# Performance work log

Measured on AMD Instinct MI355X. Metric: run time of the kernel, lower is better.

## Reference

```python
import jax, jax.numpy as jnp
import numpy as np

B, S, D, E = 2, 2048, 1024, 8
H = 2 * D          # hidden_dim = 2*n_embd
A = H // 16        # adapt_dim


def _ln(x, g, b):
    m = x.mean(-1, keepdims=True)
    v = x.var(-1, keepdims=True)
    return (x - m) * jax.lax.rsqrt(v + 1e-5) * g + b


def setup_inputs() -> dict:
    key = jax.random.key(0)
    ks = jax.random.split(key, 16)
    s = 1.0 / np.sqrt(D)        # shared-linear init scale
    sa = s * 0.01               # adapter-linear init scale
    sg = 0.01 / np.sqrt(A)      # expert adapter init scale
    f32 = jnp.float32
    return {
        "x": jax.random.normal(ks[0], (B, S, D), f32),
        "expert_weights": jax.nn.softmax(jax.random.normal(ks[1], (B * S, E), f32), -1),
        "up_w": jax.random.normal(ks[2], (H, D), f32) * s,
        "gate_w": jax.random.normal(ks[3], (H, D), f32) * s,
        "down_w": jax.random.normal(ks[4], (D, H), f32) * s,
        "pre_w": jax.random.normal(ks[5], (A, D), f32) * sa,
        "post_w": jax.random.normal(ks[6], (A, H), f32) * sa,
        "an_g": jnp.ones((A,), f32),
        "an_b": jnp.zeros((A,), f32),
        "adapt_proj_w": jax.random.normal(ks[7], (H, A), f32) * sa,
        "adapter_w": jax.random.normal(ks[8], (E, A, A), f32) * sg,
        "adapter_g": jnp.ones((E, A), f32),
        "adapter_b": jnp.zeros((E, A), f32),
        "expert_proj_w": jax.random.normal(ks[9], (H, A), f32) * sg,
        "output_proj_w": jax.random.normal(ks[10], (D, H), f32) * sg,
    }


def reference(x, expert_weights, up_w, gate_w, down_w, pre_w, post_w, an_g, an_b,
              adapt_proj_w, adapter_w, adapter_g, adapter_b, expert_proj_w, output_proj_w):
    # ---- SharedExpertMLP ----
    up = x @ up_w.T                                  # [B,S,H]
    gate = x @ gate_w.T                              # [B,S,H]
    hidden = jax.nn.silu(gate) * up                  # SwiGLU
    adapt_in = _ln(x @ pre_w.T, an_g, an_b)          # [B,S,A]
    adapt_out = _ln(hidden @ post_w.T, an_g, an_b)   # [B,S,A]
    w = jnp.einsum('bsa,bta->bst', adapt_in, adapt_out)
    w = jax.nn.silu(jnp.clip(w, -5.0, 5.0))          # clamp+SiLU score
    # explicit fp32 bmm as in original autocast-disabled block
    adapt = jnp.einsum('bst,bta->bsa',
                       w.astype(jnp.float32),
                       adapt_in.astype(jnp.float32)).astype(x.dtype)
    hidden = hidden + 0.1 * (adapt @ adapt_proj_w.T)
    shared_out = hidden @ down_w.T                   # [B,S,D] (dropout is identity in eval)

    # ---- per-token expert mixing ----
    xf = x.reshape(-1, x.shape[-1])                  # [N,D], N=B*S
    a = _ln(xf @ pre_w.T, an_g, an_b)                # [N,A]
    h = jnp.einsum('na,eca->nec', a, adapter_w)      # per-expert low-rank adapt [N,E,A]
    h = _ln(h, adapter_g[None], adapter_b[None])
    mixed = jnp.einsum('ne,nea->na', expert_weights, h)   # combine experts [N,A]
    out = (mixed @ expert_proj_w.T) @ output_proj_w.T     # [N,D]
    return shared_out + out.reshape(x.shape)
```

## Files before the change

### kernel.cpp

```cpp
#include <hip/hip_runtime.h>
#include <hip/hip_bf16.h>
#include <math.h>

#define Bq 2
#define Sq 2048
#define Dq 1024
#define Eq 8
#define Hq 2048
#define Aq 128
#define Nq (Bq*Sq)

typedef __attribute__((ext_vector_type(4))) float f32x4;
typedef __attribute__((ext_vector_type(8))) short bfrag;

__device__ __forceinline__ float silu_f(float x) {
    return x / (1.0f + expf(-x));
}
__device__ __forceinline__ unsigned short f2bf(float x) {
    unsigned u = __float_as_uint(x);
    u += 0x7fffu + ((u >> 16) & 1u);
    return (unsigned short)(u >> 16);
}
__device__ __forceinline__ float bf2f(unsigned short h) {
    return __uint_as_float(((unsigned)h) << 16);
}
__device__ __forceinline__ void gl16(const unsigned short* g, unsigned short* l) {
    __builtin_amdgcn_global_load_lds(
        (const __attribute__((address_space(1))) void*)g,
        (__attribute__((address_space(3))) void*)(void*)l, 16, 0, 0);
}

#define WAITV_BAR(N)                                            \
    asm volatile("s_waitcnt vmcnt(" #N ")" ::: "memory");       \
    __builtin_amdgcn_s_barrier();                               \
    asm volatile("" ::: "memory")
#define END_BAR()                                               \
    asm volatile("" ::: "memory");                              \
    __builtin_amdgcn_s_barrier();                               \
    asm volatile("" ::: "memory")
#define WAITV(N) asm volatile("s_waitcnt vmcnt(" #N ")" ::: "memory")
#define BARF()                                                  \
    asm volatile("" ::: "memory");                              \
    __builtin_amdgcn_s_barrier();                               \
    asm volatile("" ::: "memory")

__global__ __launch_bounds__(256)
void convert_all(const float* __restrict__ x,  const float* __restrict__ gw,
                 const float* __restrict__ uw, const float* __restrict__ dw,
                 const float* __restrict__ pw, const float* __restrict__ ow,
                 const float* __restrict__ opw, const float* __restrict__ aw,
                 const float* __restrict__ apw, const float* __restrict__ epw,
                 unsigned short* xh,  unsigned short* gwh, unsigned short* uwh,
                 unsigned short* dwh, unsigned short* pwh, unsigned short* powh,
                 unsigned short* oph, unsigned short* adw, unsigned short* apT)
{
    __shared__ float t[32][33];
    if (blockIdx.x >= 2048) {
        int bid = blockIdx.x - 2048;
        int z   = bid >> 8;
        int rem = bid & 255;
        int bx  = rem & 3, by = rem >> 2;
        const float* in = z ? epw : apw;
        unsigned short* out = apT + (size_t)z * Hq * Aq;
        int tx = threadIdx.x & 31, ty = threadIdx.x >> 5;
        int r0 = by * 32, c0 = bx * 32;
#pragma unroll
        for (int j = 0; j < 4; j++)
            t[ty + j * 8][tx] = in[(size_t)(r0 + ty + j * 8) * Aq + c0 + tx];
        __syncthreads();
#pragma unroll
        for (int j = 0; j < 4; j++)
            out[(size_t)(c0 + ty + j * 8) * Hq + r0 + tx] = f2bf(t[tx][ty + j * 8]);
        return;
    }
    const int T = 3276800;
    for (int i = blockIdx.x * 256 + threadIdx.x; i < T; i += 2048 * 256) {
        const float* in; unsigned short* hi; int j = i;
        if (j < 1048576)                 { in = x;   hi = xh;  }
        else if ((j -= 1048576) < 524288){ in = gw;  hi = gwh; }
        else if ((j -= 524288) < 524288) { in = uw;  hi = uwh; }
        else if ((j -= 524288) < 524288) { in = dw;  hi = dwh; }
        else if ((j -= 524288) < 32768)  { in = pw;  hi = pwh; }
        else if ((j -= 32768) < 65536)   { in = ow;  hi = powh; }
        else if ((j -= 65536) < 524288)  { in = opw; hi = oph; }
        else { j -= 524288;                in = aw;  hi = adw; }
        float4 v = ((const float4*)in)[j];
        ((ushort4*)hi)[j] = make_ushort4(f2bf(v.x), f2bf(v.y), f2bf(v.z), f2bf(v.w));
    }
}

template<int EPI>
__global__ __launch_bounds__(512)
void mg(const unsigned short* __restrict__ Ah, const unsigned short* __restrict__ Bh,
        void* __restrict__ Cv, int N, int K, int kchunks,
        long zA, long zB, long zC, long pz)
{
    __shared__ __align__(16) unsigned short lds[32768];

    const int tid = threadIdx.x;
    const int l   = tid & 63;
    const int w   = tid >> 6;
    const int wr  = w >> 2, wc = w & 3;
    const int bm0 = blockIdx.y * 128, bn0 = blockIdx.x * 128;
    const int bz  = blockIdx.z / kchunks;
    const int kz  = blockIdx.z - bz * kchunks;
    const int kcnt = K / kchunks;
    const int kbeg = kz * kcnt;
    const int kend = kbeg + kcnt;

    const unsigned short* A0 = Ah + (size_t)bz * zA;
    const unsigned short* B0 = Bh + (size_t)bz * zB;

    const int srow = tid >> 3;
    const int sq   = (tid & 7) ^ (srow & 7);
    const size_t aoff = (size_t)(bm0 + srow) * K + sq * 8;
    const size_t boff = (size_t)(bn0 + srow) * K + sq * 8;
    const size_t r64  = (size_t)64 * K;

    auto stage = [&](int b, int kt) {
        unsigned short* d = &lds[b * 16384 + (w << 9)];
        gl16(A0 + aoff + kt,       d + 0);
        gl16(A0 + aoff + kt + r64, d + 4096);
        gl16(B0 + boff + kt,       d + 8192);
        gl16(B0 + boff + kt + r64, d + 12288);
    };

    const int rowa = (wr * 64 + (l & 15)) * 64;
    const int rowb = (wc * 32 + (l & 15)) * 64;
    const int q0 = (((l >> 4)    ) ^ (l & 7)) << 3;
    const int q1 = (((l >> 4) + 4) ^ (l & 7)) << 3;

    f32x4 acc[4][2];
#pragma unroll
    for (int i = 0; i < 4; i++)
#pragma unroll
        for (int j = 0; j < 2; j++) acc[i][j] = (f32x4){0.f, 0.f, 0.f, 0.f};

    stage(0, kbeg);
    int cur = 0;
    for (int kt = kbeg; kt < kend; kt += 64) {
        if (kt + 64 < kend) {
            stage(cur ^ 1, kt + 64);
            WAITV_BAR(4);
        } else {
            WAITV_BAR(0);
        }
        const int cb = cur * 16384;
#pragma unroll
        for (int ks = 0; ks < 2; ks++) {
            const int qo = ks ? q1 : q0;
            bfrag a4[4], b4[2];
#pragma unroll
            for (int f = 0; f < 4; f++)
                a4[f] = *(const bfrag*)&lds[cb + rowa + f * 1024 + qo];
#pragma unroll
            for (int f = 0; f < 2; f++)
                b4[f] = *(const bfrag*)&lds[cb + 8192 + rowb + f * 1024 + qo];
#pragma unroll
            for (int i = 0; i < 4; i++)
#pragma unroll
                for (int j = 0; j < 2; j++)
                    acc[i][j] = __builtin_amdgcn_mfma_f32_16x16x32_bf16(a4[i], b4[j], acc[i][j], 0, 0, 0);
        }
        END_BAR();
        cur ^= 1;
    }

    const int crow0 = bm0 + wr * 64 + (l >> 4) * 4;
    const int ccol0 = bn0 + wc * 32 + (l & 15);
#pragma unroll
    for (int i = 0; i < 4; i++)
#pragma unroll
        for (int j = 0; j < 2; j++)
#pragma unroll
            for (int r = 0; r < 4; r++) {
                size_t idx = (size_t)(crow0 + i * 16 + r) * N + (ccol0 + j * 16);
                float v = acc[i][j][r];
                if (EPI == 0)
                    ((float*)Cv + (size_t)bz * zC + (size_t)kz * pz)[idx] = v;
                else if (EPI == 1)
                    ((unsigned short*)Cv + (size_t)bz * zC)[idx] =
                        f2bf(silu_f(fminf(fmaxf(v, -5.f), 5.f)));
                else
                    ((unsigned short*)Cv + (size_t)bz * zC)[idx] = f2bf(v);
            }
}

__global__ __launch_bounds__(512)
void mgpair(const unsigned short* __restrict__ dwh, const unsigned short* __restrict__ apT,
            float* __restrict__ kdp,
            const unsigned short* __restrict__ xh, const unsigned short* __restrict__ pwh,
            float* __restrict__ p1)
{
    __shared__ __align__(16) unsigned short lds[32768];

    const int tid = threadIdx.x;
    const int l   = tid & 63;
    const int w   = tid >> 6;
    const int wr  = w >> 2, wc = w & 3;

    const unsigned short *Ah, *Bh; float* Cv;
    int K, kchunks, by, zidx;
    long zA, zB, zC, pz;
    int bid = blockIdx.x;
    if (bid < 256) {
        Ah = dwh; Bh = apT; Cv = kdp; K = Hq; kchunks = 16;
        zA = (long)Dq * Hq; zB = (long)Aq * Hq; zC = (long)16 * Dq * Aq; pz = (long)Dq * Aq;
        by = bid & 7; zidx = bid >> 3;
    } else {
        int r = bid - 256;
        Ah = xh; Bh = pwh; Cv = p1; K = Dq; kchunks = 8;
        zA = 0; zB = 0; zC = 0; pz = (long)Nq * Aq;
        by = r & 31; zidx = r >> 5;
    }
    const int N = Aq;
    const int bm0 = by * 128, bn0 = 0;
    const int bz  = zidx / kchunks;
    const int kz  = zidx - bz * kchunks;
    const int kcnt = K / kchunks;
    const int kbeg = kz * kcnt;
    const int kend = kbeg + kcnt;

    const unsigned short* A0 = Ah + (size_t)bz * zA;
    const unsigned short* B0 = Bh + (size_t)bz * zB;

    const int srow = tid >> 3;
    const int sq   = (tid & 7) ^ (srow & 7);
    const size_t aoff = (size_t)(bm0 + srow) * K + sq * 8;
    const size_t boff = (size_t)(bn0 + srow) * K + sq * 8;
    const size_t r64  = (size_t)64 * K;

    auto stage = [&](int b, int kt) {
        unsigned short* d = &lds[b * 16384 + (w << 9)];
        gl16(A0 + aoff + kt,       d + 0);
        gl16(A0 + aoff + kt + r64, d + 4096);
        gl16(B0 + boff + kt,       d + 8192);
        gl16(B0 + boff + kt + r64, d + 12288);
    };

    const int rowa = (wr * 64 + (l & 15)) * 64;
    const int rowb = (wc * 32 + (l & 15)) * 64;
    const int q0 = (((l >> 4)    ) ^ (l & 7)) << 3;
    const int q1 = (((l >> 4) + 4) ^ (l & 7)) << 3;

    f32x4 acc[4][2];
#pragma unroll
    for (int i = 0; i < 4; i++)
#pragma unroll
        for (int j = 0; j < 2; j++) acc[i][j] = (f32x4){0.f, 0.f, 0.f, 0.f};

    stage(0, kbeg);
    int cur = 0;
    for (int kt = kbeg; kt < kend; kt += 64) {
        if (kt + 64 < kend) {
            stage(cur ^ 1, kt + 64);
            WAITV_BAR(4);
        } else {
            WAITV_BAR(0);
        }
        const int cb = cur * 16384;
#pragma unroll
        for (int ks = 0; ks < 2; ks++) {
            const int qo = ks ? q1 : q0;
            bfrag a4[4], b4[2];
#pragma unroll
            for (int f = 0; f < 4; f++)
                a4[f] = *(const bfrag*)&lds[cb + rowa + f * 1024 + qo];
#pragma unroll
            for (int f = 0; f < 2; f++)
                b4[f] = *(const bfrag*)&lds[cb + 8192 + rowb + f * 1024 + qo];
#pragma unroll
            for (int i = 0; i < 4; i++)
#pragma unroll
                for (int j = 0; j < 2; j++)
                    acc[i][j] = __builtin_amdgcn_mfma_f32_16x16x32_bf16(a4[i], b4[j], acc[i][j], 0, 0, 0);
        }
        END_BAR();
        cur ^= 1;
    }

    const int crow0 = bm0 + wr * 64 + (l >> 4) * 4;
    const int ccol0 = bn0 + wc * 32 + (l & 15);
    float* C = Cv + (size_t)bz * zC + (size_t)kz * pz;
#pragma unroll
    for (int i = 0; i < 4; i++)
#pragma unroll
        for (int j = 0; j < 2; j++)
#pragma unroll
            for (int r = 0; r < 4; r++)
                C[(size_t)(crow0 + i * 16 + r) * N + (ccol0 + j * 16)] = acc[i][j][r];
}

__global__ __launch_bounds__(512)
void gsc(const unsigned short* __restrict__ ainh, const unsigned short* __restrict__ aouth,
         const unsigned short* __restrict__ ainT, float* __restrict__ p3)
{
    __shared__ __align__(16) unsigned short lds[65536];
    const int AIN = 0, AOUT = 16384, AINT = 32768, PB = 49152;

    const int tid = threadIdx.x;
    const int l   = tid & 63;
    const int w   = tid >> 6;
    const int wr  = w >> 2, wc = w & 3;
    const int tz  = blockIdx.x;
    const int ib  = blockIdx.y;
    const int b   = blockIdx.z;
    const long SA = (long)Sq * Aq;

    auto stage32 = [&](int base, const unsigned short* src, size_t kstride) {
#pragma unroll
        for (int rd = 0; rd < 4; rd++) {
            int grow = rd * 32 + (w << 2) + (l >> 4);
            int slot = (l & 15) ^ (grow & 15);
            gl16(src + (size_t)grow * kstride + slot * 8,
                 &lds[base + rd * 4096 + (w << 9)]);
        }
    };

    const unsigned short* ainI_src = ainh + (size_t)b * SA + (size_t)(ib * 128) * Aq;
    f32x4 acc2[4][2];
#pragma unroll
    for (int i = 0; i < 4; i++)
#pragma unroll
        for (int j = 0; j < 2; j++) acc2[i][j] = (f32x4){0.f, 0.f, 0.f, 0.f};

    {
        int tglob = tz * 2;
        stage32(AIN,  ainI_src, Aq);
        stage32(AOUT, aouth + (size_t)b * SA + (size_t)(tglob * 128) * Aq, Aq);
        stage32(AINT, ainT  + (size_t)b * SA + (size_t)(tglob * 128), Sq);
        WAITV_BAR(0);
    }

    const int rowa = (wr * 64 + (l & 15)) * 128;
    const int rowb = (wc * 32 + (l & 15)) * 128;

#pragma unroll 1
    for (int t = 0; t < 2; t++) {
        if (t == 1) {
            int tglob = tz * 2 + 1;
            stage32(AOUT, aouth + (size_t)b * SA + (size_t)(tglob * 128) * Aq, Aq);
            stage32(AINT, ainT  + (size_t)b * SA + (size_t)(tglob * 128), Sq);
            WAITV_BAR(0);
        }
        f32x4 acc1[4][2];
#pragma unroll
        for (int i = 0; i < 4; i++)
#pragma unroll
            for (int j = 0; j < 2; j++) acc1[i][j] = (f32x4){0.f, 0.f, 0.f, 0.f};
#pragma unroll
        for (int ks = 0; ks < 4; ks++) {
            const int qo = ((ks * 4 + (l >> 4)) ^ (l & 15)) << 3;
            bfrag a4[4], b4[2];
#pragma unroll
            for (int f = 0; f < 4; f++)
                a4[f] = *(const bfrag*)&lds[AIN + rowa + f * 2048 + qo];
#pragma unroll
            for (int f = 0; f < 2; f++)
                b4[f] = *(const bfrag*)&lds[AOUT + rowb + f * 2048 + qo];
#pragma unroll
            for (int i = 0; i < 4; i++)
#pragma unroll
                for (int j = 0; j < 2; j++)
                    acc1[i][j] = __builtin_amdgcn_mfma_f32_16x16x32_bf16(a4[i], b4[j], acc1[i][j], 0, 0, 0);
        }
        {
            const int prow0 = wr * 64 + (l >> 4) * 4;
            const int pcol0 = wc * 32 + (l & 15);
#pragma unroll
            for (int i = 0; i < 4; i++)
#pragma unroll
                for (int j = 0; j < 2; j++)
#pragma unroll
                    for (int r = 0; r < 4; r++) {
                        int pr = prow0 + i * 16 + r;
                        int pc = pcol0 + j * 16;
                        float v = silu_f(fminf(fmaxf(acc1[i][j][r], -5.f), 5.f));
                        lds[PB + pr * 128 + (((pc >> 3) ^ (pr & 15)) << 3) + (pc & 7)] = f2bf(v);
                    }
        }
        __syncthreads();
#pragma unroll
        for (int ks = 0; ks < 4; ks++) {
            const int qo = ((ks * 4 + (l >> 4)) ^ (l & 15)) << 3;
            bfrag a4[4], b4[2];
#pragma unroll
            for (int f = 0; f < 4; f++)
                a4[f] = *(const bfrag*)&lds[PB + rowa + f * 2048 + qo];
#pragma unroll
            for (int f = 0; f < 2; f++)
                b4[f] = *(const bfrag*)&lds[AINT + rowb + f * 2048 + qo];
#pragma unroll
            for (int i = 0; i < 4; i++)
#pragma unroll
                for (int j = 0; j < 2; j++)
                    acc2[i][j] = __builtin_amdgcn_mfma_f32_16x16x32_bf16(a4[i], b4[j], acc2[i][j], 0, 0, 0);
        }
        __syncthreads();
    }

    const int crow0 = wr * 64 + (l >> 4) * 4;
    const int ccol0 = wc * 32 + (l & 15);
    float* dst = p3 + ((size_t)(b * 8 + tz) * Sq + ib * 128) * Aq;
#pragma unroll
    for (int i = 0; i < 4; i++)
#pragma unroll
        for (int j = 0; j < 2; j++)
#pragma unroll
            for (int r = 0; r < 4; r++)
                dst[(size_t)(crow0 + i * 16 + r) * Aq + ccol0 + j * 16] = acc2[i][j][r];
}

__global__ __launch_bounds__(512)
void gup(const unsigned short* __restrict__ xh, const unsigned short* __restrict__ gwh,
         const unsigned short* __restrict__ uwh, unsigned short* __restrict__ hh)
{
    __shared__ __align__(16) unsigned short lds[65536];
    const int tid = threadIdx.x;
    const int l   = tid & 63;
    const int w   = tid >> 6;
    const int wr  = w >> 2;
    const int wc  = w & 3;

    int id  = blockIdx.y * gridDim.x + blockIdx.x;
    int xcd = id & 7, j0 = id >> 3;
    int bx  = (xcd & 3) * 4 + (j0 & 3);
    int by  = (xcd >> 2) * 8 + (j0 >> 2);
    const int bm0 = by * 256, bn0 = bx * 128;

    const int srw = tid >> 3;
    const int sq  = (tid & 7) ^ (srw & 7);
    auto stageU = [&](int b, int u, int kt) {
        unsigned short* d = &lds[b * 32768 + u * 8192 + (tid << 3)];
        const unsigned short* src = (u < 2) ? xh : (u == 2 ? gwh : uwh);
        int baserow = (u < 2) ? (bm0 + u * 128) : bn0;
        size_t o = (size_t)(baserow + srw) * Dq + kt + sq * 8;
        gl16(src + o,                   d);
        gl16(src + o + (size_t)64 * Dq, d + 4096);
    };

    const int rowa = (wr * 128 + (l & 15)) * 64;
    const int rowb = (wc * 32  + (l & 15)) * 64;
    const int q0 = (((l >> 4)    ) ^ (l & 7)) << 3;
    const int q1 = (((l >> 4) + 4) ^ (l & 7)) << 3;

    f32x4 accg[8][2], accu[8][2];
#pragma unroll
    for (int i = 0; i < 8; i++)
#pragma unroll
        for (int jj = 0; jj < 2; jj++) {
            accg[i][jj] = (f32x4){0.f, 0.f, 0.f, 0.f};
            accu[i][jj] = (f32x4){0.f, 0.f, 0.f, 0.f};
        }

    stageU(0, 0, 0); stageU(0, 1, 0); stageU(0, 2, 0); stageU(0, 3, 0);
    int cur = 0;
    for (int kt = 0; kt < Dq; kt += 64) {
        const int pf = (kt + 64 < Dq);
        const int cb = cur * 32768;
        const int nx = cur ^ 1;
        bfrag a4[8], b4[2];

        WAITV(2);
        BARF();
#pragma unroll
        for (int f = 0; f < 8; f++)
            a4[f] = *(const bfrag*)&lds[cb + rowa + f * 1024 + q0];
#pragma unroll
        for (int f = 0; f < 2; f++)
            b4[f] = *(const bfrag*)&lds[cb + 16384 + rowb + f * 1024 + q0];
        if (pf) stageU(nx, 0, kt + 64);
        __builtin_amdgcn_s_setprio(1);
#pragma unroll
        for (int i = 0; i < 8; i++)
#pragma unroll
            for (int jj = 0; jj < 2; jj++)
                accg[i][jj] = __builtin_amdgcn_mfma_f32_16x16x32_bf16(a4[i], b4[jj], accg[i][jj], 0, 0, 0);
        __builtin_amdgcn_s_setprio(0);

        if (pf) { WAITV(2); } else { WAITV(0); }
        BARF();
#pragma unroll
        for (int f = 0; f < 2; f++)
            b4[f] = *(const bfrag*)&lds[cb + 24576 + rowb + f * 1024 + q0];
        if (pf) stageU(nx, 1, kt + 64);
        __builtin_amdgcn_s_setprio(1);
#pragma unroll
        for (int i = 0; i < 8; i++)
#pragma unroll
            for (int jj = 0; jj < 2; jj++)
                accu[i][jj] = __builtin_amdgcn_mfma_f32_16x16x32_bf16(a4[i], b4[jj], accu[i][jj], 0, 0, 0);
        __builtin_amdgcn_s_setprio(0);

        BARF();
#pragma unroll
        for (int f = 0; f < 8; f++)
            a4[f] = *(const bfrag*)&lds[cb + rowa + f * 1024 + q1];
#pragma unroll
        for (int f = 0; f < 2; f++)
            b4[f] = *(const bfrag*)&lds[cb + 16384 + rowb + f * 1024 + q1];
        if (pf) stageU(nx, 2, kt + 64);
        __builtin_amdgcn_s_setprio(1);
#pragma unroll
        for (int i = 0; i < 8; i++)
#pragma unroll
            for (int jj = 0; jj < 2; jj++)
                accg[i][jj] = __builtin_amdgcn_mfma_f32_16x16x32_bf16(a4[i], b4[jj], accg[i][jj], 0, 0, 0);
        __builtin_amdgcn_s_setprio(0);

        BARF();
#pragma unroll
        for (int f = 0; f < 2; f++)
            b4[f] = *(const bfrag*)&lds[cb + 24576 + rowb + f * 1024 + q1];
        if (pf) stageU(nx, 3, kt + 64);
        __builtin_amdgcn_s_setprio(1);
#pragma unroll
        for (int i = 0; i < 8; i++)
#pragma unroll
            for (int jj = 0; jj < 2; jj++)
                accu[i][jj] = __builtin_amdgcn_mfma_f32_16x16x32_bf16(a4[i], b4[jj], accu[i][jj], 0, 0, 0);
        __builtin_amdgcn_s_setprio(0);

        cur = nx;
    }

    const int crow0 = bm0 + wr * 128 + (l >> 4) * 4;
    const int ccol0 = bn0 + wc * 32 + (l & 15);
#pragma unroll
    for (int i = 0; i < 8; i++)
#pragma unroll
        for (int jj = 0; jj < 2; jj++)
#pragma unroll
            for (int r = 0; r < 4; r++) {
                size_t idx = (size_t)(crow0 + i * 16 + r) * Hq + (ccol0 + jj * 16);
                hh[idx] = f2bf(silu_f(accg[i][jj][r]) * accu[i][jj][r]);
            }
}

__global__ __launch_bounds__(512)
void gfinal(const unsigned short* __restrict__ hh, const unsigned short* __restrict__ dwh,
            const unsigned short* __restrict__ acat, const unsigned short* __restrict__ kcat,
            float* __restrict__ out)
{
    __shared__ __align__(16) unsigned short lds[49152];
    const int tid = threadIdx.x;
    const int l   = tid & 63;
    const int w   = tid >> 6;
    const int wr  = w >> 2, wc = w & 3;

    int nb  = gridDim.x * gridDim.y;
    int id  = blockIdx.y * gridDim.x + blockIdx.x;
    int id2 = (id & 7) * (nb >> 3) + (id >> 3);
    int bx  = id2 % gridDim.x, by = id2 / gridDim.x;
    const int bm0 = by * 128, bn0 = bx * 128;

    const int srow = tid >> 3;
    const int sq   = (tid & 7) ^ (srow & 7);
    const int rowa = (wr * 64 + (l & 15)) * 64;
    const int rowb = (wc * 32 + (l & 15)) * 64;
    const int q0 = (((l >> 4)    ) ^ (l & 7)) << 3;
    const int q1 = (((l >> 4) + 4) ^ (l & 7)) << 3;

    f32x4 acc[4][2];
#pragma unroll
    for (int i = 0; i < 4; i++)
#pragma unroll
        for (int j = 0; j < 2; j++) acc[i][j] = (f32x4){0.f, 0.f, 0.f, 0.f};

    {
        const size_t aoff = (size_t)(bm0 + srow) * Hq + sq * 8;
        const size_t boff = (size_t)(bn0 + srow) * Hq + sq * 8;
        const size_t r64  = (size_t)64 * Hq;
        auto stageA = [&](int b, int kt) {
            unsigned short* d = &lds[b * 16384 + (w << 9)];
            gl16(hh + aoff + kt,       d + 0);
            gl16(hh + aoff + kt + r64, d + 4096);
        };
        auto stageB = [&](int b, int kt) {
            unsigned short* d = &lds[b * 16384 + (w << 9)];
            gl16(dwh + boff + kt,       d + 8192);
            gl16(dwh + boff + kt + r64, d + 12288);
        };
        stageA(0, 0);  stageB(0, 0);
        stageA(1, 64); stageB(1, 64);
        int cur = 0;
        for (int kt = 0; kt < Hq; kt += 64) {
            if (kt + 64 < Hq) { WAITV_BAR(4); } else { WAITV_BAR(0); }
            const int pf  = (kt + 128 < Hq);
            const int nb3 = (cur + 2 >= 3) ? cur - 1 : cur + 2;
            const int cb  = cur * 16384;
            bfrag a4[4], b4[2];
#pragma unroll
            for (int f = 0; f < 4; f++)
                a4[f] = *(const bfrag*)&lds[cb + rowa + f * 1024 + q0];
#pragma unroll
            for (int f = 0; f < 2; f++)
                b4[f] = *(const bfrag*)&lds[cb + 8192 + rowb + f * 1024 + q0];
            if (pf) stageA(nb3, kt + 128);
            __builtin_amdgcn_s_setprio(1);
#pragma unroll
            for (int i = 0; i < 4; i++)
#pragma unroll
                for (int j = 0; j < 2; j++)
                    acc[i][j] = __builtin_amdgcn_mfma_f32_16x16x32_bf16(a4[i], b4[j], acc[i][j], 0, 0, 0);
            __builtin_amdgcn_s_setprio(0);
            BARF();
#pragma unroll
            for (int f = 0; f < 4; f++)
                a4[f] = *(const bfrag*)&lds[cb + rowa + f * 1024 + q1];
#pragma unroll
            for (int f = 0; f < 2; f++)
                b4[f] = *(const bfrag*)&lds[cb + 8192 + rowb + f * 1024 + q1];
            if (pf) stageB(nb3, kt + 128);
            __builtin_amdgcn_s_setprio(1);
#pragma unroll
            for (int i = 0; i < 4; i++)
#pragma unroll
                for (int j = 0; j < 2; j++)
                    acc[i][j] = __builtin_amdgcn_mfma_f32_16x16x32_bf16(a4[i], b4[j], acc[i][j], 0, 0, 0);
            __builtin_amdgcn_s_setprio(0);
            cur = (cur == 2) ? 0 : cur + 1;
        }
    }
    END_BAR();
    {
        const size_t aoff = (size_t)(bm0 + srow) * 256 + sq * 8;
        const size_t boff = (size_t)(bn0 + srow) * 256 + sq * 8;
        const size_t r64  = (size_t)64 * 256;
        auto stage2 = [&](int b, int kt) {
            unsigned short* d = &lds[b * 16384 + (w << 9)];
            gl16(acat + aoff + kt,       d + 0);
            gl16(acat + aoff + kt + r64, d + 4096);
            gl16(kcat + boff + kt,       d + 8192);
            gl16(kcat + boff + kt + r64, d + 12288);
        };
        stage2(0, 0);
        stage2(1, 64);
        int cur = 0;
        for (int kt = 0; kt < 256; kt += 64) {
            if (kt + 64 < 256) { WAITV_BAR(4); } else { WAITV_BAR(0); }
            if (kt + 128 < 256) {
                int nb3 = (cur + 2 >= 3) ? cur - 1 : cur + 2;
                stage2(nb3, kt + 128);
            }
            const int cb = cur * 16384;
#pragma unroll
            for (int ks = 0; ks < 2; ks++) {
                const int qo = ks ? q1 : q0;
                bfrag a4[4], b4[2];
#pragma unroll
                for (int f = 0; f < 4; f++)
                    a4[f] = *(const bfrag*)&lds[cb + rowa + f * 1024 + qo];
#pragma unroll
                for (int f = 0; f < 2; f++)
                    b4[f] = *(const bfrag*)&lds[cb + 8192 + rowb + f * 1024 + qo];
#pragma unroll
                for (int i = 0; i < 4; i++)
#pragma unroll
                    for (int j = 0; j < 2; j++)
                        acc[i][j] = __builtin_amdgcn_mfma_f32_16x16x32_bf16(a4[i], b4[j], acc[i][j], 0, 0, 0);
            }
            cur = (cur == 2) ? 0 : cur + 1;
        }
    }

    const int crow0 = bm0 + wr * 64 + (l >> 4) * 4;
    const int ccol0 = bn0 + wc * 32 + (l & 15);
#pragma unroll
    for (int i = 0; i < 4; i++)
#pragma unroll
        for (int j = 0; j < 2; j++)
#pragma unroll
            for (int r = 0; r < 4; r++)
                out[(size_t)(crow0 + i * 16 + r) * Dq + ccol0 + j * 16] = acc[i][j][r];
}

template<int NZ, bool WT>
__global__ __launch_bounds__(256)
void rln(const float* __restrict__ p, unsigned short* __restrict__ oh,
         unsigned short* __restrict__ aT,
         const float* __restrict__ g, const float* __restrict__ b, long pstride)
{
    int row  = blockIdx.x * 4 + (threadIdx.x >> 6);
    int lane = threadIdx.x & 63;
    long base = (long)row * Aq;
    float x0 = 0.f, x1 = 0.f;
#pragma unroll
    for (int z = 0; z < NZ; z++) {
        x0 += p[base + z * pstride + lane];
        x1 += p[base + z * pstride + lane + 64];
    }
    float s  = x0 + x1;
    float ss = x0 * x0 + x1 * x1;
#pragma unroll
    for (int off = 32; off > 0; off >>= 1) {
        s  += __shfl_xor(s, off);
        ss += __shfl_xor(ss, off);
    }
    float m  = s * (1.0f / Aq);
    float v  = ss * (1.0f / Aq) - m * m;
    float rs = rsqrtf(v + 1e-5f);
    unsigned short h0 = f2bf((x0 - m) * rs * g[lane]      + b[lane]);
    unsigned short h1 = f2bf((x1 - m) * rs * g[lane + 64] + b[lane + 64]);
    oh[base + lane]      = h0;
    oh[base + lane + 64] = h1;
    if (WT) {
        int bb2 = row >> 11, sidx = row & 2047;
        unsigned short* t = aT + (size_t)bb2 * Sq * Aq + sidx;
        t[(size_t)lane * Sq]        = h0;
        t[(size_t)(lane + 64) * Sq] = h1;
    }
}

__global__ __launch_bounds__(256)
void rlnrbf(const float* __restrict__ kdp, const float* __restrict__ p1,
            unsigned short* __restrict__ kcat,
            unsigned short* __restrict__ ainh, unsigned short* __restrict__ ainT,
            const float* __restrict__ g, const float* __restrict__ b)
{
    if (blockIdx.x < 1024) {
        int i = blockIdx.x * 256 + threadIdx.x;
        int n = i >> 7, a = i & 127;
        int bz = n >> 10, s = n & 1023;
        long base = (long)bz * 16 * Dq * Aq + (long)s * Aq + a;
        float acc = 0.f;
#pragma unroll
        for (int z = 0; z < 16; z++) acc += kdp[base + (long)z * Dq * Aq];
        kcat[(long)s * 256 + bz * 128 + a] = f2bf(acc);
        return;
    }
    int row  = (blockIdx.x - 1024) * 4 + (threadIdx.x >> 6);
    int lane = threadIdx.x & 63;
    long base = (long)row * Aq;
    float x0 = 0.f, x1 = 0.f;
#pragma unroll
    for (int z = 0; z < 8; z++) {
        x0 += p1[base + (long)z * Nq * Aq + lane];
        x1 += p1[base + (long)z * Nq * Aq + lane + 64];
    }
    float s  = x0 + x1;
    float ss = x0 * x0 + x1 * x1;
#pragma unroll
    for (int off = 32; off > 0; off >>= 1) {
        s  += __shfl_xor(s, off);
        ss += __shfl_xor(ss, off);
    }
    float m  = s * (1.0f / Aq);
    float v  = ss * (1.0f / Aq) - m * m;
    float rs = rsqrtf(v + 1e-5f);
    unsigned short h0 = f2bf((x0 - m) * rs * g[lane]      + b[lane]);
    unsigned short h1 = f2bf((x1 - m) * rs * g[lane + 64] + b[lane + 64]);
    ainh[base + lane]      = h0;
    ainh[base + lane + 64] = h1;
    int bb2 = row >> 11, sidx = row & 2047;
    unsigned short* t = ainT + (size_t)bb2 * Sq * Aq + sidx;
    t[(size_t)lane * Sq]        = h0;
    t[(size_t)(lane + 64) * Sq] = h1;
}

__global__ __launch_bounds__(256)
void tailk(const float* __restrict__ p3, const unsigned short* __restrict__ he,
           const float* __restrict__ ew, const float* __restrict__ g,
           const float* __restrict__ bb, unsigned short* __restrict__ acat)
{
    if (blockIdx.x < 2048) {
        int i = blockIdx.x * 256 + threadIdx.x;
        int n = i >> 7, a = i & 127;
        int bz = n >> 11, s = n & 2047;
        long base = ((long)bz * 8) * Sq * Aq + (long)s * Aq + a;
        float acc = 0.f;
#pragma unroll
        for (int z = 0; z < 8; z++) acc += p3[base + (long)z * Sq * Aq];
        acat[(long)n * 256 + a] = f2bf(acc * 0.1f);
        return;
    }
    int n    = (blockIdx.x - 2048) * 4 + (threadIdx.x >> 6);
    int lane = threadIdx.x & 63;
    float a0 = 0.0f, a1 = 0.0f;
#pragma unroll
    for (int e = 0; e < Eq; e++) {
        const unsigned short* r = he + ((long)e * Nq + n) * Aq;
        float x0 = bf2f(r[lane]), x1 = bf2f(r[lane + 64]);
        float s  = x0 + x1;
        float ss = x0 * x0 + x1 * x1;
#pragma unroll
        for (int off = 32; off > 0; off >>= 1) {
            s  += __shfl_xor(s, off);
            ss += __shfl_xor(ss, off);
        }
        float m  = s * (1.0f / Aq);
        float v  = ss * (1.0f / Aq) - m * m;
        float rs = rsqrtf(v + 1e-5f);
        float wv = ew[(long)n * Eq + e];
        a0 += wv * ((x0 - m) * rs * g[e * Aq + lane]      + bb[e * Aq + lane]);
        a1 += wv * ((x1 - m) * rs * g[e * Aq + lane + 64] + bb[e * Aq + lane + 64]);
    }
    acat[(long)n * 256 + 128 + lane]      = f2bf(a0);
    acat[(long)n * 256 + 128 + lane + 64] = f2bf(a1);
}

extern "C" void kernel_launch(void* const* d_in, const int* in_sizes, int n_in,
                              void* d_out, int out_size, void* d_ws, size_t ws_size,
                              hipStream_t stream)
{
    const float* x             = (const float*)d_in[0];
    const float* ew            = (const float*)d_in[1];
    const float* up_w          = (const float*)d_in[2];
    const float* gate_w        = (const float*)d_in[3];
    const float* down_w        = (const float*)d_in[4];
    const float* pre_w         = (const float*)d_in[5];
    const float* post_w        = (const float*)d_in[6];
    const float* an_g          = (const float*)d_in[7];
    const float* an_b          = (const float*)d_in[8];
    const float* adapt_proj_w  = (const float*)d_in[9];
    const float* adapter_w     = (const float*)d_in[10];
    const float* adapter_g     = (const float*)d_in[11];
    const float* adapter_b     = (const float*)d_in[12];
    const float* expert_proj_w = (const float*)d_in[13];
    const float* output_proj_w = (const float*)d_in[14];
    float* out = (float*)d_out;

#define OFF(kb) ((char*)d_ws + (size_t)(kb) * 1024)
    float* kdp  = (float*)OFF(0);
    float* p1   = (float*)OFF(16384);
    float* p2   = (float*)OFF(0);
    float* p3   = (float*)OFF(0);
    unsigned short* he = (unsigned short*)OFF(16384);
    unsigned short* hh   = (unsigned short*)OFF(32768);
    unsigned short* xh   = (unsigned short*)OFF(49152);
    unsigned short* gwh  = (unsigned short*)OFF(57344);
    unsigned short* uwh  = (unsigned short*)OFF(61440);
    unsigned short* dwh  = (unsigned short*)OFF(65536);
    unsigned short* oph  = (unsigned short*)OFF(69632);
    unsigned short* pwh  = (unsigned short*)OFF(73728);
    unsigned short* powh = (unsigned short*)OFF(73984);
    unsigned short* apT  = (unsigned short*)OFF(74496);
    unsigned short* epT  = (unsigned short*)OFF(75008);
    unsigned short* ainh = (unsigned short*)OFF(75520);
    unsigned short* ainT = (unsigned short*)OFF(76544);
    unsigned short* aouth= (unsigned short*)OFF(77568);
    unsigned short* adw  = (unsigned short*)OFF(78592);
    unsigned short* kcat = (unsigned short*)OFF(78848);
    unsigned short* acat = (unsigned short*)OFF(79360);
#undef OFF
    (void)epT;

    dim3 blk(256), blk512(512);
    const long NA = (long)Nq * Aq;

    convert_all<<<dim3(2560), blk, 0, stream>>>(x, gate_w, up_w, down_w, pre_w,
        post_w, output_proj_w, adapter_w, adapt_proj_w, expert_proj_w,
        xh, gwh, uwh, dwh, pwh, powh, oph, adw, apT);

    mgpair<<<dim3(512), blk512, 0, stream>>>(dwh, apT, kdp, xh, pwh, p1);

    rlnrbf<<<dim3(2048), blk, 0, stream>>>(kdp, p1, kcat, ainh, ainT, an_g, an_b);

    mg<2><<<dim3(1, 32, 8), blk512, 0, stream>>>(ainh, adw, he, Aq, Aq, 1,
        0, (long)Aq * Aq, NA, 0);

    gup<<<dim3(16, 16), blk512, 0, stream>>>(xh, gwh, uwh, hh);

    mg<0><<<dim3(1, 32, 8), blk512, 0, stream>>>(hh, powh, p2, Aq, Hq, 8, 0, 0, 0, NA);
    rln<8, false><<<dim3(1024), blk, 0, stream>>>(p2, aouth, nullptr, an_g, an_b, NA);

    gsc<<<dim3(8, 16, 2), blk512, 0, stream>>>(ainh, aouth, ainT, p3);

    tailk<<<dim3(3072), blk, 0, stream>>>(p3, he, ew, adapter_g, adapter_b, acat);

    gfinal<<<dim3(8, 32), blk512, 0, stream>>>(hh, dwh, acat, kcat, out);
}
```

Before: 154.0 us.

## Fuse post_w projection into gate/up GEMM epilogue with bf16 split-K partials

```diff
diff --git a/kernel.cpp b/kernel.cpp
--- a/kernel.cpp
+++ b/kernel.cpp
@@ -413,7 +413,8 @@
 
 __global__ __launch_bounds__(512)
 void gup(const unsigned short* __restrict__ xh, const unsigned short* __restrict__ gwh,
-         const unsigned short* __restrict__ uwh, unsigned short* __restrict__ hh)
+         const unsigned short* __restrict__ uwh, const unsigned short* __restrict__ powh,
+         unsigned short* __restrict__ hh, unsigned short* __restrict__ p2b)
 {
     __shared__ __align__(16) unsigned short lds[65536];
     const int tid = threadIdx.x;
@@ -524,17 +525,64 @@
         cur = nx;
     }
 
+    END_BAR();
+#pragma unroll
+    for (int rd = 0; rd < 4; rd++) {
+        int grow = rd * 32 + (w << 2) + (l >> 4);
+        int slot = (l & 15) ^ (grow & 15);
+        gl16(powh + (size_t)grow * Hq + bn0 + slot * 8,
+             &lds[32768 + rd * 4096 + (tid << 3)]);
+    }
     const int crow0 = bm0 + wr * 128 + (l >> 4) * 4;
     const int ccol0 = bn0 + wc * 32 + (l & 15);
+    const int lrow0 = wr * 128 + (l >> 4) * 4;
+    const int lcol0 = wc * 32 + (l & 15);
 #pragma unroll
     for (int i = 0; i < 8; i++)
 #pragma unroll
         for (int jj = 0; jj < 2; jj++)
 #pragma unroll
             for (int r = 0; r < 4; r++) {
-                size_t idx = (size_t)(crow0 + i * 16 + r) * Hq + (ccol0 + jj * 16);
-                hh[idx] = f2bf(silu_f(accg[i][jj][r]) * accu[i][jj][r]);
+                float hv = silu_f(accg[i][jj][r]) * accu[i][jj][r];
+                unsigned short hb = f2bf(hv);
+                hh[(size_t)(crow0 + i * 16 + r) * Hq + (ccol0 + jj * 16)] = hb;
+                int pr = lrow0 + i * 16 + r;
+                int pc = lcol0 + jj * 16;
+                lds[pr * 128 + (((pc >> 3) ^ (pr & 15)) << 3) + (pc & 7)] = hb;
             }
+    __syncthreads();
+    f32x4 acc2[8][2];
+#pragma unroll
+    for (int i = 0; i < 8; i++)
+#pragma unroll
+        for (int jj = 0; jj < 2; jj++) acc2[i][jj] = (f32x4){0.f, 0.f, 0.f, 0.f};
+    const int rowa2 = (wr * 128 + (l & 15)) * 128;
+    const int rowb2 = 32768 + (wc * 32 + (l & 15)) * 128;
+#pragma unroll
+    for (int ks = 0; ks < 4; ks++) {
+        const int qo = ((ks * 4 + (l >> 4)) ^ (l & 15)) << 3;
+        bfrag a4[8], b4[2];
+#pragma unroll
+        for (int f = 0; f < 8; f++)
+            a4[f] = *(const bfrag*)&lds[rowa2 + f * 2048 + qo];
+#pragma unroll
+        for (int f = 0; f < 2; f++)
+            b4[f] = *(const bfrag*)&lds[rowb2 + f * 2048 + qo];
+#pragma unroll
+        for (int i = 0; i < 8; i++)
+#pragma unroll
+            for (int jj = 0; jj < 2; jj++)
+                acc2[i][jj] = __builtin_amdgcn_mfma_f32_16x16x32_bf16(a4[i], b4[jj], acc2[i][jj], 0, 0, 0);
+    }
+    unsigned short* dst = p2b + (size_t)bx * Nq * Aq;
+#pragma unroll
+    for (int i = 0; i < 8; i++)
+#pragma unroll
+        for (int jj = 0; jj < 2; jj++)
+#pragma unroll
+            for (int r = 0; r < 4; r++)
+                dst[(size_t)(crow0 + i * 16 + r) * Aq + (wc * 32 + jj * 16 + (l & 15))] =
+                    f2bf(acc2[i][jj][r]);
 }
 
 __global__ __launch_bounds__(512)
@@ -675,20 +723,19 @@
                 out[(size_t)(crow0 + i * 16 + r) * Dq + ccol0 + j * 16] = acc[i][j][r];
 }
 
-template<int NZ, bool WT>
 __global__ __launch_bounds__(256)
-void rln(const float* __restrict__ p, unsigned short* __restrict__ oh,
-         unsigned short* __restrict__ aT,
-         const float* __restrict__ g, const float* __restrict__ b, long pstride)
+void rln16b(const unsigned short* __restrict__ p2b, unsigned short* __restrict__ oh,
+            const float* __restrict__ g, const float* __restrict__ b)
 {
     int row  = blockIdx.x * 4 + (threadIdx.x >> 6);
     int lane = threadIdx.x & 63;
     long base = (long)row * Aq;
+    const long PS = (long)Nq * Aq;
     float x0 = 0.f, x1 = 0.f;
 #pragma unroll
-    for (int z = 0; z < NZ; z++) {
-        x0 += p[base + z * pstride + lane];
-        x1 += p[base + z * pstride + lane + 64];
+    for (int z = 0; z < 16; z++) {
+        x0 += bf2f(p2b[base + z * PS + lane]);
+        x1 += bf2f(p2b[base + z * PS + lane + 64]);
     }
     float s  = x0 + x1;
     float ss = x0 * x0 + x1 * x1;
@@ -700,16 +747,8 @@
     float m  = s * (1.0f / Aq);
     float v  = ss * (1.0f / Aq) - m * m;
     float rs = rsqrtf(v + 1e-5f);
-    unsigned short h0 = f2bf((x0 - m) * rs * g[lane]      + b[lane]);
-    unsigned short h1 = f2bf((x1 - m) * rs * g[lane + 64] + b[lane + 64]);
-    oh[base + lane]      = h0;
-    oh[base + lane + 64] = h1;
-    if (WT) {
-        int bb2 = row >> 11, sidx = row & 2047;
-        unsigned short* t = aT + (size_t)bb2 * Sq * Aq + sidx;
-        t[(size_t)lane * Sq]        = h0;
-        t[(size_t)(lane + 64) * Sq] = h1;
-    }
+    oh[base + lane]      = f2bf((x0 - m) * rs * g[lane]      + b[lane]);
+    oh[base + lane + 64] = f2bf((x1 - m) * rs * g[lane + 64] + b[lane + 64]);
 }
 
 __global__ __launch_bounds__(256)
@@ -823,7 +862,6 @@
 #define OFF(kb) ((char*)d_ws + (size_t)(kb) * 1024)
     float* kdp  = (float*)OFF(0);
     float* p1   = (float*)OFF(16384);
-    float* p2   = (float*)OFF(0);
     float* p3   = (float*)OFF(0);
     unsigned short* he = (unsigned short*)OFF(16384);
     unsigned short* hh   = (unsigned short*)OFF(32768);
@@ -842,6 +880,7 @@
     unsigned short* adw  = (unsigned short*)OFF(78592);
     unsigned short* kcat = (unsigned short*)OFF(78848);
     unsigned short* acat = (unsigned short*)OFF(79360);
+    unsigned short* p2b  = (unsigned short*)OFF(81920);
 #undef OFF
     (void)epT;
 
@@ -859,10 +898,9 @@
     mg<2><<<dim3(1, 32, 8), blk512, 0, stream>>>(ainh, adw, he, Aq, Aq, 1,
         0, (long)Aq * Aq, NA, 0);
 
-    gup<<<dim3(16, 16), blk512, 0, stream>>>(xh, gwh, uwh, hh);
-
-    mg<0><<<dim3(1, 32, 8), blk512, 0, stream>>>(hh, powh, p2, Aq, Hq, 8, 0, 0, 0, NA);
-    rln<8, false><<<dim3(1024), blk, 0, stream>>>(p2, aouth, nullptr, an_g, an_b, NA);
+    gup<<<dim3(16, 16), blk512, 0, stream>>>(xh, gwh, uwh, powh, hh, p2b);
+
+    rln16b<<<dim3(1024), blk, 0, stream>>>(p2b, aouth, an_g, an_b);
 
     gsc<<<dim3(8, 16, 2), blk512, 0, stream>>>(ainh, aouth, ainT, p3);
 
```

Result: faster. 147.0 us (-4.5%).
